# Optimization experiments

Hardware: AMD Instinct MI355X
Metric: run time of the kernel (lower is better)

Reference implementation:

```python
import jax, jax.numpy as jnp
import numpy as np


def setup_inputs() -> dict:
    key = jax.random.key(0)
    k1, k2 = jax.random.split(key)
    x = jax.random.normal(k1, (16, 8192, 128), dtype=jnp.float32)
    embed = jax.random.normal(k2, (1024, 128), dtype=jnp.float32)
    return {"x": x, "embed": embed}


def reference(x, embed):
    # preprocess: flatten leading dims -> (N, d)
    shape = x.shape
    xf = x.reshape(-1, shape[-1])  # (N, d)
    # quantize: negative squared Euclidean distance, argmax over codebook
    dist = (2.0 * (xf @ embed.T)
            - jnp.sum(xf * xf, axis=1, keepdims=True)
            - jnp.sum(embed * embed, axis=1)[None, :])
    embed_ind = jnp.argmax(dist, axis=-1)  # (N,)
    # postprocess indices back to input leading shape
    embed_ind = embed_ind.reshape(shape[:-1])
    # dequantize: embedding lookup
    quantize = embed[embed_ind]  # (..., d)
    return embed_ind, quantize
```

## Files before the change

kernel.cpp:

```cpp
#include <hip/hip_runtime.h>
#include <math.h>


typedef __attribute__((ext_vector_type(8)))  short short8_t;
typedef __attribute__((ext_vector_type(16))) float floatx16;

constexpr int D        = 128;
constexpr int KCODES   = 1024;
constexpr int NTILES   = 32;
constexpr int ROWS_BLK = 128;
constexpr float TAU    = 0.015f;
constexpr unsigned LIST_CAP = 65536;

constexpr size_t WS_COUNTER = 0;
constexpr size_t WS_CSQ     = 256;
constexpr size_t WS_EHI     = 8192;
constexpr size_t WS_ELO     = WS_EHI + 262144;
constexpr size_t WS_LIST    = WS_ELO + 262144;
constexpr size_t WS_EMBT    = WS_LIST + 262144;

#define GLOBAL_AS __attribute__((address_space(1)))
#define LDS_AS    __attribute__((address_space(3)))

__device__ inline unsigned short bf16_rne(float v, float* back) {
    unsigned u = __float_as_uint(v);
    unsigned r = (u + 0x7FFFu + ((u >> 16) & 1u)) >> 16;
    *back = __uint_as_float(r << 16);
    return (unsigned short)r;
}

__global__ void ecb_prep(const float* __restrict__ embed, float* __restrict__ csq,
                         unsigned short* __restrict__ ehi, unsigned short* __restrict__ elo,
                         float* __restrict__ embT, unsigned int* __restrict__ counter) {
    int n = blockIdx.x * 64 + threadIdx.x;
    if (n == 0) *counter = 0u;
    if (n >= KCODES) return;
    const int t = n >> 5, nn = n & 31, nm = nn & 15;
    const float* row = embed + (size_t)n * D;
    const size_t tb = (size_t)t * 32 * D + (size_t)nn * D;
    float s = 0.f;
#pragma unroll
    for (int cc = 0; cc < 16; ++cc) {
        float4 a  = *(const float4*)(row + cc * 8);
        float4 bq = *(const float4*)(row + cc * 8 + 4);
        s = fmaf(a.x, a.x, s);  s = fmaf(a.y, a.y, s);
        s = fmaf(a.z, a.z, s);  s = fmaf(a.w, a.w, s);
        s = fmaf(bq.x, bq.x, s); s = fmaf(bq.y, bq.y, s);
        s = fmaf(bq.z, bq.z, s); s = fmaf(bq.w, bq.w, s);
        float vv[8] = {a.x, a.y, a.z, a.w, bq.x, bq.y, bq.z, bq.w};
#pragma unroll
        for (int j = 0; j < 8; ++j) embT[(size_t)(cc * 8 + j) * KCODES + n] = vv[j];
        unsigned short h[8], l[8];
#pragma unroll
        for (int j = 0; j < 8; ++j) {
            float hb, db;
            h[j] = bf16_rne(vv[j], &hb);
            l[j] = bf16_rne(vv[j] - hb, &db);
        }
        uint4 ph, pl;
        ph.x = (unsigned)h[0] | ((unsigned)h[1] << 16);
        ph.y = (unsigned)h[2] | ((unsigned)h[3] << 16);
        ph.z = (unsigned)h[4] | ((unsigned)h[5] << 16);
        ph.w = (unsigned)h[6] | ((unsigned)h[7] << 16);
        pl.x = (unsigned)l[0] | ((unsigned)l[1] << 16);
        pl.y = (unsigned)l[2] | ((unsigned)l[3] << 16);
        pl.z = (unsigned)l[4] | ((unsigned)l[5] << 16);
        pl.w = (unsigned)l[6] | ((unsigned)l[7] << 16);
        size_t dst = tb + (size_t)((cc ^ nm) * 8);
        *(uint4*)(ehi + dst) = ph;
        *(uint4*)(elo + dst) = pl;
    }
    csq[n] = s;
}

__global__ __launch_bounds__(256, 3)
void ecb_main(const float* __restrict__ x,
              const unsigned short* __restrict__ ehi, const unsigned short* __restrict__ elo,
              const float* __restrict__ csq, const float* __restrict__ embed,
              float* __restrict__ out_idx, float* __restrict__ out_q,
              unsigned int* __restrict__ counter, unsigned int* __restrict__ list) {
    __shared__ unsigned short ebuf[2][2][4096];
    __shared__ int sidx[ROWS_BLK];

    const int tid  = threadIdx.x;
    const int lane = tid & 63, wave = tid >> 6;
    const int col  = lane & 31, h = lane >> 5, colm = col & 15;
    const long rowblk = (long)blockIdx.x * ROWS_BLK;
    const int  roww   = wave * 32;

    short8_t ah[8], al[8];
    {
        const float* xr = x + (rowblk + roww + col) * (long)D + h * 8;
#pragma unroll
        for (int c = 0; c < 8; ++c) {
            float4 a  = *(const float4*)(xr + c * 16);
            float4 bq = *(const float4*)(xr + c * 16 + 4);
            float vv[8] = {a.x, a.y, a.z, a.w, bq.x, bq.y, bq.z, bq.w};
            short8_t fh, fl;
#pragma unroll
            for (int j = 0; j < 8; ++j) {
                float hb, db;
                fh[j] = (short)bf16_rne(vv[j], &hb);
                fl[j] = (short)bf16_rne(vv[j] - hb, &db);
            }
            ah[c] = fh;
            al[c] = fl;
        }
    }

    auto stage = [&](int t, int b) {
        const char* gh = (const char*)(ehi) + (size_t)t * 8192;
        const char* gl = (const char*)(elo) + (size_t)t * 8192;
        char* lh = (char*)&ebuf[b][0][0];
        char* ll = (char*)&ebuf[b][1][0];
#pragma unroll
        for (int i = 0; i < 2; ++i) {
            int off = i * 4096 + wave * 1024;
            __builtin_amdgcn_global_load_lds((const GLOBAL_AS unsigned int*)(gh + off + lane * 16),
                                             (LDS_AS unsigned int*)(lh + off), 16, 0, 0);
            __builtin_amdgcn_global_load_lds((const GLOBAL_AS unsigned int*)(gl + off + lane * 16),
                                             (LDS_AS unsigned int*)(ll + off), 16, 0, 0);
        }
    };

    float v1[16], v2[16];
#pragma unroll
    for (int j = 0; j < 16; ++j) { v1[j] = -INFINITY; v2[j] = -INFINITY; }

    stage(0, 0);
    __syncthreads();

#pragma unroll 1
    for (int t = 0; t < NTILES; ++t) {
        const int b = t & 1;
        if (t + 1 < NTILES) stage(t + 1, (t + 1) & 1);

        const float cs = csq[t * 32 + col];

        floatx16 accA, accB;
#pragma unroll
        for (int i = 0; i < 16; ++i) { accA[i] = 0.f; accB[i] = 0.f; }

#pragma unroll
        for (int s = 0; s < 8; ++s) {
            const int cc = 2 * s + h;
            const int idx = (col * 16 + (cc ^ colm)) * 8;
            short8_t bh = *(const short8_t*)&ebuf[b][0][idx];
            short8_t bl = *(const short8_t*)&ebuf[b][1][idx];
            accA = __builtin_amdgcn_mfma_f32_32x32x16_bf16(ah[s], bh, accA, 0, 0, 0);
            accB = __builtin_amdgcn_mfma_f32_32x32x16_bf16(al[s], bh, accB, 0, 0, 0);
            accB = __builtin_amdgcn_mfma_f32_32x32x16_bf16(ah[s], bl, accB, 0, 0, 0);
        }

#pragma unroll
        for (int j = 0; j < 16; ++j) {
            float sc = fmaf(2.f, accA[j] + accB[j], -cs);
            unsigned u = (__float_as_uint(sc) & ~31u) | (unsigned)t;
            float cand = __uint_as_float(u);
            float mn = fminf(v1[j], cand);
            v1[j] = fmaxf(v1[j], cand);
            v2[j] = fmaxf(v2[j], mn);
        }
        __syncthreads();
    }

#pragma unroll
    for (int j = 0; j < 16; ++j) {
        float a1 = v1[j], a2 = v2[j];
        int   c1 = ((__float_as_uint(a1) & 31u) << 5) | col;
#pragma unroll
        for (int m = 1; m < 32; m <<= 1) {
            float o1 = __shfl_xor(a1, m, 64);
            int   oc = __shfl_xor(c1, m, 64);
            float o2 = __shfl_xor(a2, m, 64);
            float lo = fminf(a1, o1);
            if (o1 > a1) { a1 = o1; c1 = oc; }
            a2 = fmaxf(fmaxf(a2, o2), lo);
        }
        if (col == j) {
            int row_local = roww + (j & 3) + 8 * (j >> 2) + 4 * h;
            long grow = rowblk + row_local;
            sidx[row_local] = c1;
            out_idx[grow] = (float)c1;
            if (a1 - a2 < TAU) {
                unsigned p = atomicAdd(counter, 1u);
                if (p < LIST_CAP) list[p] = (unsigned)grow;
            }
        }
    }
    __syncthreads();

    for (int i = tid; i < ROWS_BLK * 32; i += 256) {
        int r = i >> 5, q = i & 31;
        int code = sidx[r];
        float4 v = *(const float4*)(embed + (size_t)code * D + q * 4);
        *(float4*)(out_q + (rowblk + r) * (long)D + q * 4) = v;
    }
}

__global__ __launch_bounds__(256)
void ecb_recheck(const float* __restrict__ x, const float* __restrict__ embT,
                 const float* __restrict__ embed, const float* __restrict__ csq,
                 float* __restrict__ out_idx, float* __restrict__ out_q,
                 const unsigned int* __restrict__ counter,
                 const unsigned int* __restrict__ list) {
    __shared__ float xs[D];
    __shared__ float bv[256];
    __shared__ int   bi[256];
    const int tid = threadIdx.x;
    unsigned cnt = *counter;
    if (cnt > LIST_CAP) cnt = LIST_CAP;
    const float4* eT = (const float4*)embT;

    for (unsigned it = blockIdx.x; it < cnt; it += gridDim.x) {
        const long row = (long)list[it];
        if (tid < 32) *(float4*)&xs[tid * 4] = *(const float4*)(x + row * D + tid * 4);
        __syncthreads();

        float4 dot = {0.f, 0.f, 0.f, 0.f};
        for (int k = 0; k < D; ++k) {
            float xv = xs[k];
            float4 e = eT[(size_t)k * 256 + tid];
            dot.x = fmaf(xv, e.x, dot.x);
            dot.y = fmaf(xv, e.y, dot.y);
            dot.z = fmaf(xv, e.z, dot.z);
            dot.w = fmaf(xv, e.w, dot.w);
        }
        const int c0 = tid * 4;
        float best = -INFINITY; int bidx = 0;
        float scs[4] = {fmaf(2.f, dot.x, -csq[c0]),
                        fmaf(2.f, dot.y, -csq[c0 + 1]),
                        fmaf(2.f, dot.z, -csq[c0 + 2]),
                        fmaf(2.f, dot.w, -csq[c0 + 3])};
#pragma unroll
        for (int i = 0; i < 4; ++i)
            if (scs[i] > best) { best = scs[i]; bidx = c0 + i; }
        bv[tid] = best; bi[tid] = bidx;
        __syncthreads();
        for (int s = 128; s > 0; s >>= 1) {
            if (tid < s) {
                float ov = bv[tid + s]; int oi = bi[tid + s];
                if (ov > bv[tid] || (ov == bv[tid] && oi < bi[tid])) { bv[tid] = ov; bi[tid] = oi; }
            }
            __syncthreads();
        }
        const int win = bi[0];
        if (tid == 0) out_idx[row] = (float)win;
        if (tid < 32) {
            float4 v = *(const float4*)(embed + (size_t)win * D + tid * 4);
            *(float4*)(out_q + row * D + tid * 4) = v;
        }
        __syncthreads();
    }
}

extern "C" void kernel_launch(void* const* d_in, const int* in_sizes, int n_in,
                              void* d_out, int out_size, void* d_ws, size_t ws_size,
                              hipStream_t stream) {
    const float* x     = (const float*)d_in[0];
    const float* embed = (const float*)d_in[1];
    const int N = in_sizes[0] / D;
    char* ws = (char*)d_ws;
    unsigned int*   counter = (unsigned int*)(ws + WS_COUNTER);
    float*          csq     = (float*)(ws + WS_CSQ);
    unsigned short* ehi     = (unsigned short*)(ws + WS_EHI);
    unsigned short* elo     = (unsigned short*)(ws + WS_ELO);
    unsigned int*   list    = (unsigned int*)(ws + WS_LIST);
    float*          embT    = (float*)(ws + WS_EMBT);
    float* out_idx = (float*)d_out;
    float* out_q   = out_idx + N;

    hipLaunchKernelGGL(ecb_prep, dim3(16), dim3(64), 0, stream,
                       embed, csq, ehi, elo, embT, counter);
    hipLaunchKernelGGL(ecb_main, dim3(N / ROWS_BLK), dim3(256), 0, stream,
                       x, ehi, elo, csq, embed, out_idx, out_q, counter, list);
    hipLaunchKernelGGL(ecb_recheck, dim3(1024), dim3(256), 0, stream,
                       x, embT, embed, csq, out_idx, out_q, counter, list);
}
```

Before: 235.5 us.

## Fuse recheck into main kernel, load codebook fragments directly from global

Folds the near-tie recheck into the main kernel using a per-block shared-memory list, so the separate recheck launch and the global atomic counter are gone. The codebook staging through double-buffered LDS is replaced by direct global loads of pre-swizzled bf16 fragments laid out per MFMA lane. The factor of 2 is folded into the x split and the negated norms seed the accumulator, and the prep kernel is widened to more threads with a shuffle-based norm reduction. Occupancy hint drops from 3 to 2 blocks per CU. The risks are exposed global-load latency without LDS pipelining, and blocks with many ambiguous rows serialising the scalar recheck.

```diff
diff --git a/kernel.cpp b/kernel.cpp
--- a/kernel.cpp
+++ b/kernel.cpp
@@ -10,17 +10,11 @@
 constexpr int NTILES   = 32;
 constexpr int ROWS_BLK = 128;
 constexpr float TAU    = 0.015f;
-constexpr unsigned LIST_CAP = 65536;
-
-constexpr size_t WS_COUNTER = 0;
-constexpr size_t WS_CSQ     = 256;
-constexpr size_t WS_EHI     = 8192;
-constexpr size_t WS_ELO     = WS_EHI + 262144;
-constexpr size_t WS_LIST    = WS_ELO + 262144;
-constexpr size_t WS_EMBT    = WS_LIST + 262144;
-
-#define GLOBAL_AS __attribute__((address_space(1)))
-#define LDS_AS    __attribute__((address_space(3)))
+
+constexpr size_t WS_NCSQ = 0;
+constexpr size_t WS_EHI  = 4096;
+constexpr size_t WS_ELO  = WS_EHI + 262144;
+constexpr size_t WS_EMBT = WS_ELO + 262144;
 
 __device__ inline unsigned short bf16_rne(float v, float* back) {
     unsigned u = __float_as_uint(v);
@@ -29,64 +23,67 @@
     return (unsigned short)r;
 }
 
-__global__ void ecb_prep(const float* __restrict__ embed, float* __restrict__ csq,
-                         unsigned short* __restrict__ ehi, unsigned short* __restrict__ elo,
-                         float* __restrict__ embT, unsigned int* __restrict__ counter) {
-    int n = blockIdx.x * 64 + threadIdx.x;
-    if (n == 0) *counter = 0u;
-    if (n >= KCODES) return;
-    const int t = n >> 5, nn = n & 31, nm = nn & 15;
-    const float* row = embed + (size_t)n * D;
-    const size_t tb = (size_t)t * 32 * D + (size_t)nn * D;
-    float s = 0.f;
-#pragma unroll
-    for (int cc = 0; cc < 16; ++cc) {
-        float4 a  = *(const float4*)(row + cc * 8);
-        float4 bq = *(const float4*)(row + cc * 8 + 4);
-        s = fmaf(a.x, a.x, s);  s = fmaf(a.y, a.y, s);
-        s = fmaf(a.z, a.z, s);  s = fmaf(a.w, a.w, s);
-        s = fmaf(bq.x, bq.x, s); s = fmaf(bq.y, bq.y, s);
-        s = fmaf(bq.z, bq.z, s); s = fmaf(bq.w, bq.w, s);
-        float vv[8] = {a.x, a.y, a.z, a.w, bq.x, bq.y, bq.z, bq.w};
-#pragma unroll
-        for (int j = 0; j < 8; ++j) embT[(size_t)(cc * 8 + j) * KCODES + n] = vv[j];
-        unsigned short h[8], l[8];
-#pragma unroll
-        for (int j = 0; j < 8; ++j) {
-            float hb, db;
-            h[j] = bf16_rne(vv[j], &hb);
-            l[j] = bf16_rne(vv[j] - hb, &db);
-        }
-        uint4 ph, pl;
-        ph.x = (unsigned)h[0] | ((unsigned)h[1] << 16);
-        ph.y = (unsigned)h[2] | ((unsigned)h[3] << 16);
-        ph.z = (unsigned)h[4] | ((unsigned)h[5] << 16);
-        ph.w = (unsigned)h[6] | ((unsigned)h[7] << 16);
-        pl.x = (unsigned)l[0] | ((unsigned)l[1] << 16);
-        pl.y = (unsigned)l[2] | ((unsigned)l[3] << 16);
-        pl.z = (unsigned)l[4] | ((unsigned)l[5] << 16);
-        pl.w = (unsigned)l[6] | ((unsigned)l[7] << 16);
-        size_t dst = tb + (size_t)((cc ^ nm) * 8);
-        *(uint4*)(ehi + dst) = ph;
-        *(uint4*)(elo + dst) = pl;
-    }
-    csq[n] = s;
-}
-
-__global__ __launch_bounds__(256, 3)
+__global__ __launch_bounds__(256)
+void ecb_prep(const float* __restrict__ embed, float* __restrict__ ncsq,
+              unsigned short* __restrict__ ehi, unsigned short* __restrict__ elo,
+              float* __restrict__ embT) {
+    const int tid = threadIdx.x;
+    const int cc = tid & 15;
+    const int nl = tid >> 4;
+    const int n  = blockIdx.x * 16 + nl;
+    const int t = n >> 5, nn = n & 31;
+    const float* src = embed + (size_t)n * D + cc * 8;
+    float4 a = *(const float4*)src;
+    float4 b = *(const float4*)(src + 4);
+    float vv[8] = {a.x, a.y, a.z, a.w, b.x, b.y, b.z, b.w};
+    float ss = 0.f;
+    unsigned short hq[8], lq[8];
+#pragma unroll
+    for (int j = 0; j < 8; ++j) {
+        ss = fmaf(vv[j], vv[j], ss);
+        float hb, db;
+        hq[j] = bf16_rne(vv[j], &hb);
+        lq[j] = bf16_rne(vv[j] - hb, &db);
+    }
+    uint4 ph, pl;
+    ph.x = (unsigned)hq[0] | ((unsigned)hq[1] << 16);
+    ph.y = (unsigned)hq[2] | ((unsigned)hq[3] << 16);
+    ph.z = (unsigned)hq[4] | ((unsigned)hq[5] << 16);
+    ph.w = (unsigned)hq[6] | ((unsigned)hq[7] << 16);
+    pl.x = (unsigned)lq[0] | ((unsigned)lq[1] << 16);
+    pl.y = (unsigned)lq[2] | ((unsigned)lq[3] << 16);
+    pl.z = (unsigned)lq[4] | ((unsigned)lq[5] << 16);
+    pl.w = (unsigned)lq[6] | ((unsigned)lq[7] << 16);
+    size_t dst = ((size_t)(t * 8 + (cc >> 1)) * 64 + (size_t)((cc & 1) * 32 + nn)) * 8;
+    *(uint4*)(ehi + dst) = ph;
+    *(uint4*)(elo + dst) = pl;
+#pragma unroll
+    for (int j = 0; j < 8; ++j) embT[(size_t)(cc * 8 + j) * KCODES + n] = vv[j];
+#pragma unroll
+    for (int m = 1; m < 16; m <<= 1) ss += __shfl_xor(ss, m, 64);
+    if (cc == 0) ncsq[n] = -ss;
+}
+
+__global__ __launch_bounds__(256, 2)
 void ecb_main(const float* __restrict__ x,
               const unsigned short* __restrict__ ehi, const unsigned short* __restrict__ elo,
-              const float* __restrict__ csq, const float* __restrict__ embed,
-              float* __restrict__ out_idx, float* __restrict__ out_q,
-              unsigned int* __restrict__ counter, unsigned int* __restrict__ list) {
-    __shared__ unsigned short ebuf[2][2][4096];
-    __shared__ int sidx[ROWS_BLK];
+              const float* __restrict__ ncsq, const float* __restrict__ embed,
+              const float* __restrict__ embT,
+              float* __restrict__ out_idx, float* __restrict__ out_q) {
+    __shared__ int   sidx[ROWS_BLK];
+    __shared__ unsigned char llist[ROWS_BLK];
+    __shared__ unsigned lcount;
+    __shared__ float xs[D];
+    __shared__ float bv[256];
+    __shared__ int   bi[256];
 
     const int tid  = threadIdx.x;
     const int lane = tid & 63, wave = tid >> 6;
-    const int col  = lane & 31, h = lane >> 5, colm = col & 15;
+    const int col  = lane & 31, h = lane >> 5;
     const long rowblk = (long)blockIdx.x * ROWS_BLK;
     const int  roww   = wave * 32;
+
+    if (tid == 0) lcount = 0u;
 
     short8_t ah[8], al[8];
     {
@@ -94,80 +91,64 @@
 #pragma unroll
         for (int c = 0; c < 8; ++c) {
             float4 a  = *(const float4*)(xr + c * 16);
-            float4 bq = *(const float4*)(xr + c * 16 + 4);
-            float vv[8] = {a.x, a.y, a.z, a.w, bq.x, bq.y, bq.z, bq.w};
+            float4 b  = *(const float4*)(xr + c * 16 + 4);
+            float vv[8] = {a.x, a.y, a.z, a.w, b.x, b.y, b.z, b.w};
             short8_t fh, fl;
 #pragma unroll
             for (int j = 0; j < 8; ++j) {
+                float v2x = vv[j] + vv[j];
                 float hb, db;
-                fh[j] = (short)bf16_rne(vv[j], &hb);
-                fl[j] = (short)bf16_rne(vv[j] - hb, &db);
+                fh[j] = (short)bf16_rne(v2x, &hb);
+                fl[j] = (short)bf16_rne(v2x - hb, &db);
             }
             ah[c] = fh;
             al[c] = fl;
         }
     }
 
-    auto stage = [&](int t, int b) {
-        const char* gh = (const char*)(ehi) + (size_t)t * 8192;
-        const char* gl = (const char*)(elo) + (size_t)t * 8192;
-        char* lh = (char*)&ebuf[b][0][0];
-        char* ll = (char*)&ebuf[b][1][0];
-#pragma unroll
-        for (int i = 0; i < 2; ++i) {
-            int off = i * 4096 + wave * 1024;
-            __builtin_amdgcn_global_load_lds((const GLOBAL_AS unsigned int*)(gh + off + lane * 16),
-                                             (LDS_AS unsigned int*)(lh + off), 16, 0, 0);
-            __builtin_amdgcn_global_load_lds((const GLOBAL_AS unsigned int*)(gl + off + lane * 16),
-                                             (LDS_AS unsigned int*)(ll + off), 16, 0, 0);
-        }
-    };
-
     float v1[16], v2[16];
 #pragma unroll
     for (int j = 0; j < 16; ++j) { v1[j] = -INFINITY; v2[j] = -INFINITY; }
 
-    stage(0, 0);
+    const short8_t* Bh = (const short8_t*)ehi + lane;
+    const short8_t* Bl = (const short8_t*)elo + lane;
+
     __syncthreads();
 
 #pragma unroll 1
     for (int t = 0; t < NTILES; ++t) {
-        const int b = t & 1;
-        if (t + 1 < NTILES) stage(t + 1, (t + 1) & 1);
-
-        const float cs = csq[t * 32 + col];
-
+        const float negcs = ncsq[t * 32 + col];
+        short8_t bh[8], bl[8];
+#pragma unroll
+        for (int s = 0; s < 8; ++s) {
+            bh[s] = Bh[(size_t)(t * 8 + s) * 64];
+            bl[s] = Bl[(size_t)(t * 8 + s) * 64];
+        }
         floatx16 accA, accB;
 #pragma unroll
-        for (int i = 0; i < 16; ++i) { accA[i] = 0.f; accB[i] = 0.f; }
-
+        for (int i = 0; i < 16; ++i) { accA[i] = negcs; accB[i] = 0.f; }
 #pragma unroll
         for (int s = 0; s < 8; ++s) {
-            const int cc = 2 * s + h;
-            const int idx = (col * 16 + (cc ^ colm)) * 8;
-            short8_t bh = *(const short8_t*)&ebuf[b][0][idx];
-            short8_t bl = *(const short8_t*)&ebuf[b][1][idx];
-            accA = __builtin_amdgcn_mfma_f32_32x32x16_bf16(ah[s], bh, accA, 0, 0, 0);
-            accB = __builtin_amdgcn_mfma_f32_32x32x16_bf16(al[s], bh, accB, 0, 0, 0);
-            accB = __builtin_amdgcn_mfma_f32_32x32x16_bf16(ah[s], bl, accB, 0, 0, 0);
-        }
-
+            accA = __builtin_amdgcn_mfma_f32_32x32x16_bf16(ah[s], bh[s], accA, 0, 0, 0);
+            accB = __builtin_amdgcn_mfma_f32_32x32x16_bf16(al[s], bh[s], accB, 0, 0, 0);
+            accB = __builtin_amdgcn_mfma_f32_32x32x16_bf16(ah[s], bl[s], accB, 0, 0, 0);
+        }
 #pragma unroll
         for (int j = 0; j < 16; ++j) {
-            float sc = fmaf(2.f, accA[j] + accB[j], -cs);
+            float sc = accA[j] + accB[j];
             unsigned u = (__float_as_uint(sc) & ~31u) | (unsigned)t;
             float cand = __uint_as_float(u);
             float mn = fminf(v1[j], cand);
             v1[j] = fmaxf(v1[j], cand);
             v2[j] = fmaxf(v2[j], mn);
         }
-        __syncthreads();
+        __builtin_amdgcn_s_barrier();
     }
 
 #pragma unroll
     for (int j = 0; j < 16; ++j) {
         float a1 = v1[j], a2 = v2[j];
-        int   c1 = ((__float_as_uint(a1) & 31u) << 5) | col;
+        int   c1 = (int)((__float_as_uint(a1) & 31u) << 5) | col;
 #pragma unroll
         for (int m = 1; m < 32; m <<= 1) {
             float o1 = __shfl_xor(a1, m, 64);
@@ -179,12 +160,11 @@
         }
         if (col == j) {
             int row_local = roww + (j & 3) + 8 * (j >> 2) + 4 * h;
-            long grow = rowblk + row_local;
             sidx[row_local] = c1;
-            out_idx[grow] = (float)c1;
+            out_idx[rowblk + row_local] = (float)c1;
             if (a1 - a2 < TAU) {
-                unsigned p = atomicAdd(counter, 1u);
-                if (p < LIST_CAP) list[p] = (unsigned)grow;
+                unsigned p = atomicAdd(&lcount, 1u);
+                llist[p] = (unsigned char)row_local;
             }
         }
     }
@@ -193,31 +173,20 @@
     for (int i = tid; i < ROWS_BLK * 32; i += 256) {
         int r = i >> 5, q = i & 31;
         int code = sidx[r];
-        float4 v = *(const float4*)(embed + (size_t)code * D + q * 4);
-        *(float4*)(out_q + (rowblk + r) * (long)D + q * 4) = v;
-    }
-}
-
-__global__ __launch_bounds__(256)
-void ecb_recheck(const float* __restrict__ x, const float* __restrict__ embT,
-                 const float* __restrict__ embed, const float* __restrict__ csq,
-                 float* __restrict__ out_idx, float* __restrict__ out_q,
-                 const unsigned int* __restrict__ counter,
-                 const unsigned int* __restrict__ list) {
-    __shared__ float xs[D];
-    __shared__ float bv[256];
-    __shared__ int   bi[256];
-    const int tid = threadIdx.x;
-    unsigned cnt = *counter;
-    if (cnt > LIST_CAP) cnt = LIST_CAP;
+        float4 ev = *(const float4*)(embed + (size_t)code * D + q * 4);
+        *(float4*)(out_q + (rowblk + r) * (long)D + q * 4) = ev;
+    }
+    __syncthreads();
+
+    const unsigned nf = lcount;
     const float4* eT = (const float4*)embT;
-
-    for (unsigned it = blockIdx.x; it < cnt; it += gridDim.x) {
-        const long row = (long)list[it];
+    for (unsigned f = 0; f < nf; ++f) {
+        const int rl  = llist[f];
+        const long row = rowblk + rl;
         if (tid < 32) *(float4*)&xs[tid * 4] = *(const float4*)(x + row * D + tid * 4);
         __syncthreads();
-
         float4 dot = {0.f, 0.f, 0.f, 0.f};
+#pragma unroll 8
         for (int k = 0; k < D; ++k) {
             float xv = xs[k];
             float4 e = eT[(size_t)k * 256 + tid];
@@ -227,11 +196,11 @@
             dot.w = fmaf(xv, e.w, dot.w);
         }
         const int c0 = tid * 4;
+        float scs[4] = {fmaf(2.f, dot.x, ncsq[c0]),
+                        fmaf(2.f, dot.y, ncsq[c0 + 1]),
+                        fmaf(2.f, dot.z, ncsq[c0 + 2]),
+                        fmaf(2.f, dot.w, ncsq[c0 + 3])};
         float best = -INFINITY; int bidx = 0;
-        float scs[4] = {fmaf(2.f, dot.x, -csq[c0]),
-                        fmaf(2.f, dot.y, -csq[c0 + 1]),
-                        fmaf(2.f, dot.z, -csq[c0 + 2]),
-                        fmaf(2.f, dot.w, -csq[c0 + 3])};
 #pragma unroll
         for (int i = 0; i < 4; ++i)
             if (scs[i] > best) { best = scs[i]; bidx = c0 + i; }
@@ -247,8 +216,8 @@
         const int win = bi[0];
         if (tid == 0) out_idx[row] = (float)win;
         if (tid < 32) {
-            float4 v = *(const float4*)(embed + (size_t)win * D + tid * 4);
-            *(float4*)(out_q + row * D + tid * 4) = v;
+            float4 ev = *(const float4*)(embed + (size_t)win * D + tid * 4);
+            *(float4*)(out_q + row * D + tid * 4) = ev;
         }
         __syncthreads();
     }
@@ -261,19 +230,15 @@
     const float* embed = (const float*)d_in[1];
     const int N = in_sizes[0] / D;
     char* ws = (char*)d_ws;
-    unsigned int*   counter = (unsigned int*)(ws + WS_COUNTER);
-    float*          csq     = (float*)(ws + WS_CSQ);
-    unsigned short* ehi     = (unsigned short*)(ws + WS_EHI);
-    unsigned short* elo     = (unsigned short*)(ws + WS_ELO);
-    unsigned int*   list    = (unsigned int*)(ws + WS_LIST);
-    float*          embT    = (float*)(ws + WS_EMBT);
+    float*          ncsq = (float*)(ws + WS_NCSQ);
+    unsigned short* ehi  = (unsigned short*)(ws + WS_EHI);
+    unsigned short* elo  = (unsigned short*)(ws + WS_ELO);
+    float*          embT = (float*)(ws + WS_EMBT);
     float* out_idx = (float*)d_out;
     float* out_q   = out_idx + N;
 
-    hipLaunchKernelGGL(ecb_prep, dim3(16), dim3(64), 0, stream,
-                       embed, csq, ehi, elo, embT, counter);
+    hipLaunchKernelGGL(ecb_prep, dim3(64), dim3(256), 0, stream,
+                       embed, ncsq, ehi, elo, embT);
     hipLaunchKernelGGL(ecb_main, dim3(N / ROWS_BLK), dim3(256), 0, stream,
-                       x, ehi, elo, csq, embed, out_idx, out_q, counter, list);
-    hipLaunchKernelGGL(ecb_recheck, dim3(1024), dim3(256), 0, stream,
-                       x, embT, embed, csq, out_idx, out_q, counter, list);
-}
+                       x, ehi, elo, ncsq, embed, embT, out_idx, out_q);
+}
```

New measurement: 249.4 us. 5.9% more time.
